# Performance work log

Measured on AMD Instinct MI355X. Metric: run time of the kernel, lower is better.

The kernel has to match this reference:

```python
import jax, jax.numpy as jnp
import numpy as np

COMMITMENT_COST = 0.25


def setup_inputs() -> dict:
    key = jax.random.key(0)
    k1, k2 = jax.random.split(key, 2)
    inputs = jax.random.normal(k1, (8, 2048, 1024), dtype=jnp.float32)
    # per-head codebooks: [H=4, K=1024, dh=256]
    codebook = jax.random.normal(k2, (4, 1024, 256), dtype=jnp.float32)
    return {"inputs": inputs, "codebook": codebook}


def reference(inputs, codebook):
    H, K, dh = codebook.shape
    flat = inputs.reshape(-1, H, dh)  # [N, H, dh]
    # squared-euclidean distances per head: [H, N, K]
    x_sq = jnp.sum(flat * flat, axis=-1).T[:, :, None]          # [H, N, 1]
    c_sq = jnp.sum(codebook * codebook, axis=-1)[:, None, :]    # [H, 1, K]
    dots = jnp.einsum('nhd,hkd->hnk', flat, codebook)           # [H, N, K]
    distances = x_sq + c_sq - 2.0 * dots
    idx = jnp.argmin(distances, axis=-1)                        # [H, N]
    # gather codebook rows (equivalent to one-hot @ codebook)
    q = jnp.take_along_axis(codebook, idx[:, :, None], axis=1)  # [H, N, dh]
    quantized = jnp.transpose(q, (1, 0, 2)).reshape(inputs.shape)
    # ema=True, eval mode: q_latent_loss = 0
    e_latent_loss = jnp.mean((jax.lax.stop_gradient(quantized) - inputs) ** 2)
    loss = COMMITMENT_COST * e_latent_loss
    # residual=False: straight-through estimator
    quantized_out = inputs + jax.lax.stop_gradient(quantized - inputs)
    return loss, quantized_out
```

## Files before the change

### kernel.cpp

```cpp
#include <hip/hip_runtime.h>
#include <cfloat>

#define NH    4
#define NK    1024
#define DHD   256
#define NTOK  16384
#define ROWS  (NH * DHD)

typedef __attribute__((ext_vector_type(8))) short bf16x8;
typedef __attribute__((ext_vector_type(4))) float f32x4;

#define WS_CSQ  ((size_t)0)
#define WS_BH   ((size_t)16384)
#define WS_BL   (WS_BH + (size_t)2097152)
#define WS_CAND (WS_BL + (size_t)2097152)
#define WS_NEED (WS_CAND + (size_t)524288)

__device__ __forceinline__ unsigned short f32_to_bf16_rn(float f) {
    unsigned u = __float_as_uint(f);
    u += 0x7FFFu + ((u >> 16) & 1u);
    return (unsigned short)(u >> 16);
}
__device__ __forceinline__ float bf16_as_f32(unsigned short h) {
    return __uint_as_float(((unsigned)h) << 16);
}

__device__ __forceinline__ void gload_lds16(const uint4* g, uint4* l) {
    __builtin_amdgcn_global_load_lds(
        (const __attribute__((address_space(1))) void*)g,
        (__attribute__((address_space(3))) void*)l, 16, 0, 0);
}

__global__ __launch_bounds__(64) void csq_kernel(const float* __restrict__ cb,
                                                 float* __restrict__ csq) {
    const int code = blockIdx.x;
    const int lane = threadIdx.x;
    const float4 v = *(const float4*)(cb + (size_t)code * DHD + lane * 4);
    float s = v.x * v.x + v.y * v.y + v.z * v.z + v.w * v.w;
#pragma unroll
    for (int off = 32; off > 0; off >>= 1) s += __shfl_down(s, off, 64);
    if (lane == 0) csq[code] = s;
}

__global__ __launch_bounds__(256) void cvt_cb_kernel(const float* __restrict__ cb,
                                                     uint4* __restrict__ bch,
                                                     uint4* __restrict__ bcl) {
    const int g = blockIdx.x * 8 + (threadIdx.x >> 5);
    const int o = threadIdx.x & 31;
    const float* src = cb + (size_t)g * DHD + o * 8;
    unsigned wh[4], wl[4];
#pragma unroll
    for (int i = 0; i < 4; ++i) {
        const float f0 = src[2 * i], f1 = src[2 * i + 1];
        const unsigned short h0 = f32_to_bf16_rn(f0);
        const unsigned short h1 = f32_to_bf16_rn(f1);
        const unsigned short l0 = f32_to_bf16_rn(f0 - bf16_as_f32(h0));
        const unsigned short l1 = f32_to_bf16_rn(f1 - bf16_as_f32(h1));
        wh[i] = (unsigned)h0 | ((unsigned)h1 << 16);
        wl[i] = (unsigned)l0 | ((unsigned)l1 << 16);
    }
    const int hh = g >> 10, c = g & 1023, dc = o >> 2, kk = o & 3;
    const size_t unit = (size_t)((hh * 8 + dc) * 4 + kk) * NK + c;
    bch[unit] = make_uint4(wh[0], wh[1], wh[2], wh[3]);
    bcl[unit] = make_uint4(wl[0], wl[1], wl[2], wl[3]);
}

__device__ __forceinline__ bool lt_vi(float v, int i, float w, int j) {
    return (v < w) || (v == w && i < j);
}

__device__ __forceinline__ float np_sq_pairwise256(const float* __restrict__ a) {
#pragma clang fp contract(off)
    float tot = 0.f;
#pragma unroll
    for (int blk = 0; blk < 2; ++blk) {
        const float* p = a + blk * 128;
        float r0 = p[0] * p[0], r1 = p[1] * p[1], r2 = p[2] * p[2], r3 = p[3] * p[3];
        float r4 = p[4] * p[4], r5 = p[5] * p[5], r6 = p[6] * p[6], r7 = p[7] * p[7];
#pragma clang loop unroll_count(2)
        for (int i = 8; i < 128; i += 8) {
            r0 = r0 + p[i + 0] * p[i + 0];
            r1 = r1 + p[i + 1] * p[i + 1];
            r2 = r2 + p[i + 2] * p[i + 2];
            r3 = r3 + p[i + 3] * p[i + 3];
            r4 = r4 + p[i + 4] * p[i + 4];
            r5 = r5 + p[i + 5] * p[i + 5];
            r6 = r6 + p[i + 6] * p[i + 6];
            r7 = r7 + p[i + 7] * p[i + 7];
        }
        const float res = ((r0 + r1) + (r2 + r3)) + ((r4 + r5) + (r6 + r7));
        tot = (blk == 0) ? res : (tot + res);
    }
    return tot;
}

__device__ __forceinline__ float np_dot_seq256(const float* __restrict__ a,
                                               const float* __restrict__ b) {
#pragma clang fp contract(off)
    float s = 0.f;
#pragma clang loop unroll_count(4)
    for (int i = 0; i < 256; ++i) s = s + a[i] * b[i];
    return s;
}

__device__ __forceinline__ void refine_exact(const float* __restrict__ xr,
                                             const float* __restrict__ cr,
                                             float& Xo, float& Co, float& Do) {
#pragma clang fp contract(off)
    float s = 0.f;
    float X = 0.f, C = 0.f;
    for (int blk = 0; blk < 2; ++blk) {
        const float4* xq = (const float4*)(xr + blk * 128);
        const float4* cq = (const float4*)(cr + blk * 128);
        float xa[8], ca[8];
#pragma unroll
        for (int j = 0; j < 8; ++j) { xa[j] = 0.f; ca[j] = 0.f; }
#pragma clang loop unroll_count(4)
        for (int g = 0; g < 16; ++g) {
            const float4 a0 = xq[2 * g], a1 = xq[2 * g + 1];
            const float4 b0 = cq[2 * g], b1 = cq[2 * g + 1];
            const float xf[8] = {a0.x, a0.y, a0.z, a0.w, a1.x, a1.y, a1.z, a1.w};
            const float cf[8] = {b0.x, b0.y, b0.z, b0.w, b1.x, b1.y, b1.z, b1.w};
#pragma unroll
            for (int j = 0; j < 8; ++j) {
                xa[j] = xa[j] + xf[j] * xf[j];
                ca[j] = ca[j] + cf[j] * cf[j];
            }
#pragma unroll
            for (int j = 0; j < 8; ++j) s = s + xf[j] * cf[j];
        }
        const float xres = ((xa[0] + xa[1]) + (xa[2] + xa[3])) + ((xa[4] + xa[5]) + (xa[6] + xa[7]));
        const float cres = ((ca[0] + ca[1]) + (ca[2] + ca[3])) + ((ca[4] + ca[5]) + (ca[6] + ca[7]));
        X = (blk == 0) ? xres : (X + xres);
        C = (blk == 0) ? cres : (C + cres);
    }
    Xo = X; Co = C; Do = s;
}

__global__ __launch_bounds__(256, 2) void vq_mfma(const float* __restrict__ x,
                                                  const float* __restrict__ csq,
                                                  const uint4* __restrict__ bch,
                                                  const uint4* __restrict__ bcl,
                                                  int* __restrict__ candw) {
    __shared__ uint4 BsH[2048];
    __shared__ uint4 BsL[2048];
    __shared__ float Cs[NK];

    const int tid  = threadIdx.x;
    const int h    = blockIdx.y;
    const int t0   = blockIdx.x * 128;
    const int wv   = tid >> 6;
    const int lane = tid & 63;
    const int kk   = lane >> 4;
    const int ln   = lane & 15;

#pragma unroll
    for (int i = tid; i < NK; i += 256) Cs[i] = csq[h * NK + i];

    bf16x8 aH[2][8], aL[2][8];
    {
        const int tokb = t0 + wv * 32 + ln;
        const float* xa = x + (size_t)tokb * ROWS + h * DHD + kk * 8;
#pragma unroll
        for (int rt = 0; rt < 2; ++rt) {
#pragma unroll
            for (int dc = 0; dc < 8; ++dc) {
                const float* p = xa + (size_t)(rt * 16) * ROWS + dc * 32;
                const float4 f0 = *(const float4*)p;
                const float4 f1 = *(const float4*)(p + 4);
                const float f[8] = {f0.x, f0.y, f0.z, f0.w, f1.x, f1.y, f1.z, f1.w};
                bf16x8 hv, lv;
#pragma unroll
                for (int j = 0; j < 8; ++j) {
                    const unsigned short hb = f32_to_bf16_rn(f[j]);
                    hv[j] = (short)hb;
                    lv[j] = (short)f32_to_bf16_rn(f[j] - bf16_as_f32(hb));
                }
                aH[rt][dc] = hv;
                aL[rt][dc] = lv;
            }
        }
    }

    float b1[8], b2[8];
    int   i1[8], i2[8];
#pragma unroll
    for (int s = 0; s < 8; ++s) { b1[s] = FLT_MAX; b2[s] = FLT_MAX; i1[s] = 0; i2[s] = 0; }

    for (int k0 = 0; k0 < NK; k0 += 64) {
        __syncthreads();
#pragma unroll
        for (int p = 0; p < 8; ++p) {
            const size_t w = (size_t)(h * 32 + p * 4 + wv) * NK + k0 + lane;
            gload_lds16(&bch[w], &BsH[p * 256 + wv * 64]);
            gload_lds16(&bcl[w], &BsL[p * 256 + wv * 64]);
        }
        __syncthreads();

        f32x4 acc[2][4];
#pragma unroll
        for (int rt = 0; rt < 2; ++rt)
#pragma unroll
            for (int ct = 0; ct < 4; ++ct) acc[rt][ct] = (f32x4){0.f, 0.f, 0.f, 0.f};

#pragma unroll
        for (int dc = 0; dc < 8; ++dc) {
#pragma unroll
            for (int ct = 0; ct < 4; ++ct) {
                const int bu = (dc * 4 + kk) * 64 + ct * 16 + ln;
                const bf16x8 bH = *(const bf16x8*)&BsH[bu];
                const bf16x8 bL = *(const bf16x8*)&BsL[bu];
#pragma unroll
                for (int rt = 0; rt < 2; ++rt) {
                    acc[rt][ct] = __builtin_amdgcn_mfma_f32_16x16x32_bf16(aH[rt][dc], bH, acc[rt][ct], 0, 0, 0);
                    acc[rt][ct] = __builtin_amdgcn_mfma_f32_16x16x32_bf16(aH[rt][dc], bL, acc[rt][ct], 0, 0, 0);
                    acc[rt][ct] = __builtin_amdgcn_mfma_f32_16x16x32_bf16(aL[rt][dc], bH, acc[rt][ct], 0, 0, 0);
                }
            }
        }

#pragma unroll
        for (int rt = 0; rt < 2; ++rt)
#pragma unroll
            for (int ct = 0; ct < 4; ++ct) {
                const float cs   = Cs[k0 + ct * 16 + ln];
                const int   codg = k0 + ct * 16 + ln;
#pragma unroll
                for (int r = 0; r < 4; ++r) {
                    const float dist = cs - 2.f * acc[rt][ct][r];
                    const int   s    = rt * 4 + r;
                    if (dist < b1[s]) { b2[s] = b1[s]; i2[s] = i1[s]; b1[s] = dist; i1[s] = codg; }
                    else if (dist < b2[s]) { b2[s] = dist; i2[s] = codg; }
                }
            }
    }

#pragma unroll
    for (int s = 0; s < 8; ++s) {
        float v1 = b1[s], v2 = b2[s];
        int   j1 = i1[s], j2 = i2[s];
#pragma unroll
        for (int m = 1; m <= 8; m <<= 1) {
            const float o1 = __shfl_xor(v1, m, 64);
            const int   oj1 = __shfl_xor(j1, m, 64);
            const float o2 = __shfl_xor(v2, m, 64);
            const int   oj2 = __shfl_xor(j2, m, 64);
            if (lt_vi(o1, oj1, v1, j1)) {
                if (lt_vi(v1, j1, o2, oj2)) { v2 = v1; j2 = j1; }
                else                        { v2 = o2; j2 = oj2; }
                v1 = o1; j1 = oj1;
            } else if (lt_vi(o1, oj1, v2, j2)) {
                v2 = o1; j2 = oj1;
            }
        }
        if (ln == 0) {
            const int tl  = wv * 32 + (s >> 2) * 16 + kk * 4 + (s & 3);
            const int gid = h * NTOK + t0 + tl;
            candw[2 * gid + 0] = j1;
            candw[2 * gid + 1] = j2;
        }
    }
}

__global__ __launch_bounds__(64) void vq_tail(const float* __restrict__ x,
                                              const float* __restrict__ cb,
                                              const int* __restrict__ candw,
                                              float* __restrict__ out) {
    const int lane = threadIdx.x;
    const int rowb = blockIdx.x * 32;
    const int h    = rowb >> 14;
    const int tb   = rowb & (NTOK - 1);
    const float* cbh = cb + (size_t)h * NK * DHD;

    const int rloc = lane >> 1;
    const int cand = lane & 1;
    const int row  = rowb + rloc;
    const int t    = tb + rloc;
    const int code = candw[2 * row + cand];
    const float* xr = x + (size_t)t * ROWS + h * DHD;
    const float* cr = cbh + (size_t)code * DHD;
    float X, C, D;
    refine_exact(xr, cr, X, C, D);
    float d;
    {
#pragma clang fp contract(off)
        const float tt = X + C;
        d = tt - 2.0f * D;
    }
    const float od = __shfl_xor(d, 1, 64);
    int sel = code;
    if (cand == 0) {
        const int jB = candw[2 * row + 1];
        const bool pickB = (od < d) || (od == d && jB < code);
        if (pickB) sel = jB;
    }

    float lacc = 0.f;
    for (int r = 0; r < 32; ++r) {
        const int cr_code = __shfl(sel, 2 * r, 64);
        const int tr = tb + r;
        const float4 q4 = *(const float4*)(cbh + (size_t)cr_code * DHD + (lane << 2));
        const float4 x4 = *(const float4*)(x + (size_t)tr * ROWS + h * DHD + (lane << 2));
        const float dx = q4.x - x4.x, dy = q4.y - x4.y;
        const float dz = q4.z - x4.z, dw = q4.w - x4.w;
        lacc += dx * dx + dy * dy + dz * dz + dw * dw;
        *(float4*)(out + 1 + (size_t)tr * ROWS + h * DHD + (lane << 2)) = q4;
    }
#pragma unroll
    for (int off = 32; off > 0; off >>= 1) lacc += __shfl_down(lacc, off, 64);
    if (lane == 0) atomicAdd(out, lacc * (0.25f / 16777216.f));
}

#define TN 128
#define TK 128
#define KC 16
#define APAD 4
#define BPAD 4

__global__ __launch_bounds__(256, 2) void vq_main_fp32(const float* __restrict__ x,
                                                       const float* __restrict__ cb,
                                                       const float* __restrict__ csq,
                                                       float* __restrict__ out) {
    __shared__ float As[KC][TN + APAD];
    __shared__ float Bs[KC][TK + BPAD];
    __shared__ float Cs[TK];
    __shared__ int   Cand[TN][2];
    __shared__ int   SIdx[TN];
    __shared__ float WSum[4];

    const int tid = threadIdx.x;
    const int h   = blockIdx.y;
    const int t0  = blockIdx.x * TN;
    const int ty  = tid >> 4;
    const int tx  = tid & 15;

    const float* xh  = x  + (size_t)t0 * ROWS + h * DHD;
    const float* cbh = cb + (size_t)h * NK * DHD;

    const int sr = tid >> 1;
    const int sd = (tid & 1) << 3;

    float b1[8], b2[8];
    int   i1[8], i2[8];
#pragma unroll
    for (int r = 0; r < 8; ++r) { b1[r] = FLT_MAX; b2[r] = FLT_MAX; i1[r] = 0; i2[r] = 0; }

    for (int k0 = 0; k0 < NK; k0 += TK) {
        __syncthreads();
        if (tid < TK) Cs[tid] = csq[h * NK + k0 + tid];

        float acc[8][8];
#pragma unroll
        for (int r = 0; r < 8; ++r)
#pragma unroll
            for (int c = 0; c < 8; ++c) acc[r][c] = 0.f;

        for (int d0 = 0; d0 < DHD; d0 += KC) {
            __syncthreads();
            {
                const float* ap = xh + (size_t)sr * ROWS + d0 + sd;
                const float4 a0 = *(const float4*)ap;
                const float4 a1 = *(const float4*)(ap + 4);
                As[sd + 0][sr] = a0.x; As[sd + 1][sr] = a0.y;
                As[sd + 2][sr] = a0.z; As[sd + 3][sr] = a0.w;
                As[sd + 4][sr] = a1.x; As[sd + 5][sr] = a1.y;
                As[sd + 6][sr] = a1.z; As[sd + 7][sr] = a1.w;
            }
            {
                const float* bp = cbh + (size_t)(k0 + sr) * DHD + d0 + sd;
                const float4 b0v = *(const float4*)bp;
                const float4 b1v = *(const float4*)(bp + 4);
                Bs[sd + 0][sr] = b0v.x; Bs[sd + 1][sr] = b0v.y;
                Bs[sd + 2][sr] = b0v.z; Bs[sd + 3][sr] = b0v.w;
                Bs[sd + 4][sr] = b1v.x; Bs[sd + 5][sr] = b1v.y;
                Bs[sd + 6][sr] = b1v.z; Bs[sd + 7][sr] = b1v.w;
            }
            __syncthreads();
#pragma unroll 4
            for (int kc = 0; kc < KC; ++kc) {
                const float4 a0 = *(const float4*)&As[kc][ty << 3];
                const float4 a1 = *(const float4*)&As[kc][(ty << 3) + 4];
                const float4 p0 = *(const float4*)&Bs[kc][tx << 2];
                const float4 p1 = *(const float4*)&Bs[kc][64 + (tx << 2)];
                const float aa[8] = {a0.x, a0.y, a0.z, a0.w, a1.x, a1.y, a1.z, a1.w};
                const float bb[8] = {p0.x, p0.y, p0.z, p0.w, p1.x, p1.y, p1.z, p1.w};
#pragma unroll
                for (int r = 0; r < 8; ++r)
#pragma unroll
                    for (int c = 0; c < 8; ++c)
                        acc[r][c] = fmaf(aa[r], bb[c], acc[r][c]);
            }
        }
#pragma unroll
        for (int r = 0; r < 8; ++r) {
#pragma unroll
            for (int c = 0; c < 8; ++c) {
                const int cc = (c < 4) ? ((tx << 2) + c) : (64 + (tx << 2) + c - 4);
                const float dist = Cs[cc] - 2.f * acc[r][c];
                const int   idx  = k0 + cc;
                if (dist < b1[r]) { b2[r] = b1[r]; i2[r] = i1[r]; b1[r] = dist; i1[r] = idx; }
                else if (dist < b2[r]) { b2[r] = dist; i2[r] = idx; }
            }
        }
    }

#pragma unroll
    for (int r = 0; r < 8; ++r) {
        float v1 = b1[r], v2 = b2[r];
        int   j1 = i1[r], j2 = i2[r];
#pragma unroll
        for (int m = 1; m <= 8; m <<= 1) {
            const float o1 = __shfl_xor(v1, m, 64);
            const int   oj1 = __shfl_xor(j1, m, 64);
            const float o2 = __shfl_xor(v2, m, 64);
            const int   oj2 = __shfl_xor(j2, m, 64);
            if (lt_vi(o1, oj1, v1, j1)) {
                if (lt_vi(v1, j1, o2, oj2)) { v2 = v1; j2 = j1; }
                else                        { v2 = o2; j2 = oj2; }
                v1 = o1; j1 = oj1;
            } else if (lt_vi(o1, oj1, v2, j2)) {
                v2 = o1; j2 = oj1;
            }
        }
        b1[r] = v1; i1[r] = j1; b2[r] = v2; i2[r] = j2;
    }
    if (tx == 0) {
#pragma unroll
        for (int r = 0; r < 8; ++r) {
            Cand[(ty << 3) + r][0] = i1[r];
            Cand[(ty << 3) + r][1] = i2[r];
        }
    }
    __syncthreads();

    {
        const int token = tid >> 1;
        const int cand  = tid & 1;
        const int code  = Cand[token][cand];
        const float* xr = xh + (size_t)token * ROWS;
        const float* cr = cbh + (size_t)code * DHD;
        const float X = np_sq_pairwise256(xr);
        const float C = np_sq_pairwise256(cr);
        const float D = np_dot_seq256(xr, cr);
        float d;
        {
#pragma clang fp contract(off)
            const float t = X + C;
            d = t - 2.0f * D;
        }
        const float od = __shfl_xor(d, 1, 64);
        if (cand == 0) {
            const int jA = code;
            const int jB = Cand[token][1];
            const bool pickB = (od < d) || (od == d && jB < jA);
            SIdx[token] = pickB ? jB : jA;
        }
    }
    __syncthreads();

    const int wav  = tid >> 6;
    const int lane = tid & 63;
    float lacc = 0.f;
    for (int t = wav; t < TN; t += 4) {
        const float4 q4 = *(const float4*)(cbh + (size_t)SIdx[t] * DHD + (lane << 2));
        const float4 x4 = *(const float4*)(xh + (size_t)t * ROWS + (lane << 2));
        const float dx = q4.x - x4.x, dy = q4.y - x4.y;
        const float dz = q4.z - x4.z, dw = q4.w - x4.w;
        lacc += dx * dx + dy * dy + dz * dz + dw * dw;
        *(float4*)(out + 1 + (size_t)(t0 + t) * ROWS + h * DHD + (lane << 2)) = q4;
    }
#pragma unroll
    for (int off = 32; off > 0; off >>= 1) lacc += __shfl_down(lacc, off, 64);
    if (lane == 0) WSum[wav] = lacc;
    __syncthreads();
    if (tid == 0) {
        const float s = WSum[0] + WSum[1] + WSum[2] + WSum[3];
        atomicAdd(out, s * (0.25f / 16777216.f));
    }
}

extern "C" void kernel_launch(void* const* d_in, const int* in_sizes, int n_in,
                              void* d_out, int out_size, void* d_ws, size_t ws_size,
                              hipStream_t stream) {
    const float* x   = (const float*)d_in[0];
    const float* cb  = (const float*)d_in[1];
    float*       out = (float*)d_out;
    char*        ws  = (char*)d_ws;
    float*       csq = (float*)(ws + WS_CSQ);

    hipMemsetAsync(d_out, 0, sizeof(float), stream);
    csq_kernel<<<NH * NK, 64, 0, stream>>>(cb, csq);

    if (ws_size >= WS_NEED) {
        uint4* bch   = (uint4*)(ws + WS_BH);
        uint4* bcl   = (uint4*)(ws + WS_BL);
        int*   candw = (int*)(ws + WS_CAND);
        cvt_cb_kernel<<<NH * NK / 8, 256, 0, stream>>>(cb, bch, bcl);
        dim3 grid(NTOK / 128, NH);
        vq_mfma<<<grid, 256, 0, stream>>>(x, csq, bch, bcl, candw);
        vq_tail<<<NTOK * NH / 32, 64, 0, stream>>>(x, cb, candw, out);
    } else {
        dim3 grid(NTOK / TN, NH);
        vq_main_fp32<<<grid, 256, 0, stream>>>(x, cb, csq, out);
    }
}
```

Measured before the change: 324.0 us.

## Fuse codebook norms into conversion, shrink MFMA code tile, reuse refine distance for loss

Computes the per-code squared norms inside the bf16 split conversion kernel, which removes the separate csq launch on the MFMA path. The MFMA kernel's code tile shrinks from 64 to 32 codes per iteration. That halves LDS staging and the accumulator registers but doubles the number of barrier-synchronised iterations. The tail kernel now takes the loss term from the exact refined distance of the chosen code instead of rereading x and recomputing (q-x)^2. This saves a global read of the inputs, but the expanded x^2+c^2-2xc form can differ slightly in rounding from the direct squared difference.

```diff
diff --git a/kernel.cpp b/kernel.cpp
--- a/kernel.cpp
+++ b/kernel.cpp
@@ -44,14 +44,17 @@
 
 __global__ __launch_bounds__(256) void cvt_cb_kernel(const float* __restrict__ cb,
                                                      uint4* __restrict__ bch,
-                                                     uint4* __restrict__ bcl) {
+                                                     uint4* __restrict__ bcl,
+                                                     float* __restrict__ csq) {
     const int g = blockIdx.x * 8 + (threadIdx.x >> 5);
     const int o = threadIdx.x & 31;
     const float* src = cb + (size_t)g * DHD + o * 8;
     unsigned wh[4], wl[4];
+    float s = 0.f;
 #pragma unroll
     for (int i = 0; i < 4; ++i) {
         const float f0 = src[2 * i], f1 = src[2 * i + 1];
+        s += f0 * f0 + f1 * f1;
         const unsigned short h0 = f32_to_bf16_rn(f0);
         const unsigned short h1 = f32_to_bf16_rn(f1);
         const unsigned short l0 = f32_to_bf16_rn(f0 - bf16_as_f32(h0));
@@ -63,6 +66,9 @@
     const size_t unit = (size_t)((hh * 8 + dc) * 4 + kk) * NK + c;
     bch[unit] = make_uint4(wh[0], wh[1], wh[2], wh[3]);
     bcl[unit] = make_uint4(wl[0], wl[1], wl[2], wl[3]);
+#pragma unroll
+    for (int m = 16; m > 0; m >>= 1) s += __shfl_xor(s, m, 32);
+    if (o == 0) csq[g] = s;
 }
 
 __device__ __forceinline__ bool lt_vi(float v, int i, float w, int j) {
@@ -137,13 +143,16 @@
     Xo = X; Co = C; Do = s;
 }
 
+#define KT 32
+#define NTIL (NK / KT)
+
 __global__ __launch_bounds__(256, 2) void vq_mfma(const float* __restrict__ x,
                                                   const float* __restrict__ csq,
                                                   const uint4* __restrict__ bch,
                                                   const uint4* __restrict__ bcl,
                                                   int* __restrict__ candw) {
-    __shared__ uint4 BsH[2048];
-    __shared__ uint4 BsL[2048];
+    __shared__ uint4 BsH[1024];
+    __shared__ uint4 BsL[1024];
     __shared__ float Cs[NK];
 
     const int tid  = threadIdx.x;
@@ -187,27 +196,30 @@
 #pragma unroll
     for (int s = 0; s < 8; ++s) { b1[s] = FLT_MAX; b2[s] = FLT_MAX; i1[s] = 0; i2[s] = 0; }
 
-    for (int k0 = 0; k0 < NK; k0 += 64) {
+    for (int t = 0; t < NTIL; ++t) {
+        const int k0 = t * KT;
         __syncthreads();
 #pragma unroll
-        for (int p = 0; p < 8; ++p) {
-            const size_t w = (size_t)(h * 32 + p * 4 + wv) * NK + k0 + lane;
-            gload_lds16(&bch[w], &BsH[p * 256 + wv * 64]);
-            gload_lds16(&bcl[w], &BsL[p * 256 + wv * 64]);
+        for (int p = 0; p < 4; ++p) {
+            const int q   = wv * 4 + p;
+            const int row = 2 * q + (lane >> 5);
+            const size_t w = (size_t)(h * 32 + row) * NK + k0 + (lane & 31);
+            gload_lds16(&bch[w], &BsH[q * 64]);
+            gload_lds16(&bcl[w], &BsL[q * 64]);
         }
         __syncthreads();
 
-        f32x4 acc[2][4];
+        f32x4 acc[2][2];
 #pragma unroll
         for (int rt = 0; rt < 2; ++rt)
 #pragma unroll
-            for (int ct = 0; ct < 4; ++ct) acc[rt][ct] = (f32x4){0.f, 0.f, 0.f, 0.f};
+            for (int ct = 0; ct < 2; ++ct) acc[rt][ct] = (f32x4){0.f, 0.f, 0.f, 0.f};
 
 #pragma unroll
         for (int dc = 0; dc < 8; ++dc) {
 #pragma unroll
-            for (int ct = 0; ct < 4; ++ct) {
-                const int bu = (dc * 4 + kk) * 64 + ct * 16 + ln;
+            for (int ct = 0; ct < 2; ++ct) {
+                const int bu = (dc * 4 + kk) * 32 + ct * 16 + ln;
                 const bf16x8 bH = *(const bf16x8*)&BsH[bu];
                 const bf16x8 bL = *(const bf16x8*)&BsL[bu];
 #pragma unroll
@@ -222,7 +234,7 @@
 #pragma unroll
         for (int rt = 0; rt < 2; ++rt)
 #pragma unroll
-            for (int ct = 0; ct < 4; ++ct) {
+            for (int ct = 0; ct < 2; ++ct) {
                 const float cs   = Cs[k0 + ct * 16 + ln];
                 const int   codg = k0 + ct * 16 + ln;
 #pragma unroll
@@ -288,22 +300,19 @@
         d = tt - 2.0f * D;
     }
     const float od = __shfl_xor(d, 1, 64);
-    int sel = code;
+    int   sel  = code;
+    float lacc = 0.f;
     if (cand == 0) {
         const int jB = candw[2 * row + 1];
         const bool pickB = (od < d) || (od == d && jB < code);
-        if (pickB) sel = jB;
-    }
-
-    float lacc = 0.f;
+        sel  = pickB ? jB : code;
+        lacc = pickB ? od : d;
+    }
+
     for (int r = 0; r < 32; ++r) {
         const int cr_code = __shfl(sel, 2 * r, 64);
         const int tr = tb + r;
         const float4 q4 = *(const float4*)(cbh + (size_t)cr_code * DHD + (lane << 2));
-        const float4 x4 = *(const float4*)(x + (size_t)tr * ROWS + h * DHD + (lane << 2));
-        const float dx = q4.x - x4.x, dy = q4.y - x4.y;
-        const float dz = q4.z - x4.z, dw = q4.w - x4.w;
-        lacc += dx * dx + dy * dy + dz * dz + dw * dw;
         *(float4*)(out + 1 + (size_t)tr * ROWS + h * DHD + (lane << 2)) = q4;
     }
 #pragma unroll
@@ -489,17 +498,17 @@
     float*       csq = (float*)(ws + WS_CSQ);
 
     hipMemsetAsync(d_out, 0, sizeof(float), stream);
-    csq_kernel<<<NH * NK, 64, 0, stream>>>(cb, csq);
 
     if (ws_size >= WS_NEED) {
         uint4* bch   = (uint4*)(ws + WS_BH);
         uint4* bcl   = (uint4*)(ws + WS_BL);
         int*   candw = (int*)(ws + WS_CAND);
-        cvt_cb_kernel<<<NH * NK / 8, 256, 0, stream>>>(cb, bch, bcl);
+        cvt_cb_kernel<<<NH * NK / 8, 256, 0, stream>>>(cb, bch, bcl, csq);
         dim3 grid(NTOK / 128, NH);
         vq_mfma<<<grid, 256, 0, stream>>>(x, csq, bch, bcl, candw);
         vq_tail<<<NTOK * NH / 32, 64, 0, stream>>>(x, cb, candw, out);
     } else {
+        csq_kernel<<<NH * NK, 64, 0, stream>>>(cb, csq);
         dim3 grid(NTOK / TN, NH);
         vq_main_fp32<<<grid, 256, 0, stream>>>(x, cb, csq, out);
     }
```

New measurement: 308.2 us. 4.9% less time.
